# Performance work log

Measured on AMD Instinct MI355X. Metric: run time of the kernel, lower is better.

The kernel has to match this reference:

```python
import jax, jax.numpy as jnp
import numpy as np

NH, NW = 5, 5          # attn_neighborhood_size (odd -> symmetric 'same' padding)
HEADS, HEAD_DIM = 8, 64
DIM = 512              # == heads*head_dim, but project_out=True since heads>1
B, HMAP, WMAP = 4, 64, 64
N = HMAP * WMAP


def local_expand(t, height, width):
    """Equivalent of impulse-filter conv2d neighbor gather.

    t: [b, heads, n, d] -> [b, heads, n, NH*NW, d]
    neighbor f=(i,j) of pixel (p,q) is t[p+i-NH//2, q+j-NW//2], zero-padded.
    """
    b, h, n, d = t.shape
    y = t.reshape(b, h, height, width, d)
    ph, pw = NH // 2, NW // 2
    yp = jnp.pad(y, ((0, 0), (0, 0), (ph, ph), (pw, pw), (0, 0)))
    # fixed small loop over the 25 window offsets (row-major = filter order)
    slabs = [yp[:, :, i:i + height, j:j + width, :]
             for i in range(NH) for j in range(NW)]
    out = jnp.stack(slabs, axis=4)  # [b, h, H, W, F, d]
    return out.reshape(b, h, n, NH * NW, d)


def setup_inputs() -> dict:
    key = jax.random.key(0)
    k1, k2, k3, k4 = jax.random.split(key, 4)
    inner = HEADS * HEAD_DIM
    x = jax.random.normal(k1, (B, N, DIM), dtype=jnp.float32)
    # torch Linear weights are [out_features, in_features]
    w_qkv = jax.random.normal(k2, (3 * inner, DIM), dtype=jnp.float32) * (DIM ** -0.5)
    w_out = jax.random.normal(k3, (DIM, inner), dtype=jnp.float32) * (inner ** -0.5)
    b_out = jax.random.normal(k4, (DIM,), dtype=jnp.float32) * 0.01
    return {"x": x, "w_qkv": w_qkv, "w_out": w_out, "b_out": b_out,
            "h": HMAP, "w": WMAP}


def reference(x, w_qkv, w_out, b_out, h, w):
    b, n, _ = x.shape
    scale = HEAD_DIM ** -0.5
    qkv = x @ w_qkv.T                                   # [b, n, 3*inner]
    q, k, v = jnp.split(qkv, 3, axis=-1)
    def to_heads(t):
        return t.reshape(b, n, HEADS, HEAD_DIM).transpose(0, 2, 1, 3)  # b h n d
    q, k, v = to_heads(q), to_heads(k), to_heads(v)
    k_loc = local_expand(k, h, w)                       # [b, h, n, F, d]
    v_loc = local_expand(v, h, w)
    dots = jnp.einsum('bhnd,bhnfd->bhnf', q, k_loc) * scale
    attn = jax.nn.softmax(dots, axis=-1)
    out = jnp.einsum('bhnf,bhnfd->bhnd', attn, v_loc)   # [b, h, n, d]
    out = out.transpose(0, 2, 1, 3).reshape(b, n, HEADS * HEAD_DIM)
    return out @ w_out.T + b_out                        # dropout=0 (eval)
```

## Files before the change

kernel.cpp:

```cpp
#include <hip/hip_runtime.h>
#include <cstddef>
#include <cstdint>


namespace {

typedef short s16x8 __attribute__((ext_vector_type(8)));
typedef unsigned short u16x8 __attribute__((ext_vector_type(8)));
typedef float f32x4 __attribute__((ext_vector_type(4)));

constexpr int kHeads = 8;
constexpr int kN = 4096;
constexpr float kScale = 0.125f;

__device__ inline float b2f(unsigned short u) {
  return __uint_as_float((unsigned)u << 16);
}
__device__ inline unsigned short f2b(float x) {
  unsigned u = __float_as_uint(x);
  return (unsigned short)((u + 0x7fffu + ((u >> 16) & 1u)) >> 16);
}

__device__ __forceinline__ void g2l16(const unsigned short* g,
                                      unsigned short* l) {
  __builtin_amdgcn_global_load_lds(
      (const __attribute__((address_space(1))) void*)g,
      (__attribute__((address_space(3))) void*)l, 16, 0, 0);
}

__global__ __launch_bounds__(256) void cvt_all(
    const float* __restrict__ wq, const float* __restrict__ wo,
    const float* __restrict__ x, unsigned short* __restrict__ wqb,
    unsigned short* __restrict__ wob, unsigned short* __restrict__ xb) {
  const int i = blockIdx.x * 256 + threadIdx.x;
  const float* src;
  unsigned short* dst;
  int off;
  if (i < 98304) {
    src = wq; dst = wqb; off = i;
  } else if (i < 131072) {
    src = wo; dst = wob; off = i - 98304;
  } else {
    src = x; dst = xb; off = i - 131072;
  }
  const float4 a = ((const float4*)src)[off * 2];
  const float4 b = ((const float4*)src)[off * 2 + 1];
  u16x8 o;
  o[0] = f2b(a.x); o[1] = f2b(a.y); o[2] = f2b(a.z); o[3] = f2b(a.w);
  o[4] = f2b(b.x); o[5] = f2b(b.y); o[6] = f2b(b.z); o[7] = f2b(b.w);
  *(u16x8*)(dst + (size_t)off * 8) = o;
}

__device__ __forceinline__ void mfma_512(const unsigned short* __restrict__ A,
                                         const unsigned short* __restrict__ W,
                                         int m0, int n0, int tid,
                                         unsigned short* As, unsigned short* Bs,
                                         f32x4 (&acc)[4][4]) {
  const int lane = tid & 63;
  const int wv = tid >> 6;
  const int wm = wv & 1, wn = wv >> 1;
  const int rsub = lane >> 3;
  const int slog = (lane & 7) ^ rsub;
#pragma unroll
  for (int i = 0; i < 4; ++i)
#pragma unroll
    for (int j = 0; j < 4; ++j) acc[i][j] = f32x4{0.f, 0.f, 0.f, 0.f};

  for (int k0 = 0; k0 < 512; k0 += 64) {
#pragma unroll
    for (int it = 0; it < 4; ++it) {
      const int g = wv * 4 + it;
      const int row = g * 8 + rsub;
      g2l16(A + (size_t)(m0 + row) * 512 + k0 + slog * 8, As + g * 512);
      g2l16(W + (size_t)(n0 + row) * 512 + k0 + slog * 8, Bs + g * 512);
    }
    __syncthreads();
#pragma unroll
    for (int kh = 0; kh < 2; ++kh) {
      s16x8 af[4], bf[4];
      const int q = kh * 4 + (lane >> 4);
#pragma unroll
      for (int i = 0; i < 4; ++i) {
        const int Ra = wm * 64 + i * 16 + (lane & 15);
        af[i] = *(const s16x8*)&As[Ra * 64 + ((q ^ (Ra & 7)) * 8)];
        const int Rb = wn * 64 + i * 16 + (lane & 15);
        bf[i] = *(const s16x8*)&Bs[Rb * 64 + ((q ^ (Rb & 7)) * 8)];
      }
#pragma unroll
      for (int i = 0; i < 4; ++i)
#pragma unroll
        for (int j = 0; j < 4; ++j)
          acc[i][j] = __builtin_amdgcn_mfma_f32_16x16x32_bf16(
              af[i], bf[j], acc[i][j], 0, 0, 0);
    }
    __syncthreads();
  }
}

__global__ __launch_bounds__(256, 3) void gemm_qkv(
    const unsigned short* __restrict__ A, const unsigned short* __restrict__ W,
    unsigned short* __restrict__ Qb, unsigned short* __restrict__ Kb,
    unsigned short* __restrict__ Vb) {
  __shared__ unsigned short As[8192], Bs[8192];
  const int tid = threadIdx.x;
  const int id = blockIdx.x;
  const int xcd = id & 7;
  const int j = id >> 3;
  const int by = xcd * 16 + j / 12;
  const int bx = j % 12;
  f32x4 acc[4][4];
  mfma_512(A, W, by * 128, bx * 128, tid, As, Bs, acc);

  const int lane = tid & 63;
  const int wv = tid >> 6;
  const int wm = wv & 1, wn = wv >> 1;
  const int cn = bx * 128 + wn * 64;
  unsigned short* dst = (cn < 512) ? Qb : (cn < 1024 ? Kb : Vb);
  const int head = (cn >> 6) & 7;
  const int colb = lane & 15;
#pragma unroll
  for (int mi = 0; mi < 4; ++mi) {
#pragma unroll
    for (int r = 0; r < 4; ++r) {
      const int m = by * 128 + wm * 64 + mi * 16 + (lane >> 4) * 4 + r;
      const int b = m >> 12;
      const int p = m & 4095;
      unsigned short* o =
          dst + ((size_t)(b * kHeads + head) * kN + p) * 64 + colb;
#pragma unroll
      for (int ni = 0; ni < 4; ++ni) o[ni * 16] = f2b(acc[mi][ni][r]);
    }
  }
}

__global__ __launch_bounds__(256, 3) void gemm_out(
    const unsigned short* __restrict__ A, const unsigned short* __restrict__ W,
    const float* __restrict__ bias, float* __restrict__ out) {
  __shared__ unsigned short As[8192], Bs[8192];
  const int tid = threadIdx.x;
  const int id = blockIdx.x;
  const int xcd = id & 7;
  const int j = id >> 3;
  const int by = xcd * 16 + (j >> 2);
  const int bx = j & 3;
  f32x4 acc[4][4];
  mfma_512(A, W, by * 128, bx * 128, tid, As, Bs, acc);

  const int lane = tid & 63;
  const int wv = tid >> 6;
  const int wm = wv & 1, wn = wv >> 1;
  float bvr[4];
#pragma unroll
  for (int ni = 0; ni < 4; ++ni)
    bvr[ni] = bias[bx * 128 + wn * 64 + ni * 16 + (lane & 15)];
#pragma unroll
  for (int mi = 0; mi < 4; ++mi) {
#pragma unroll
    for (int r = 0; r < 4; ++r) {
      const int m = by * 128 + wm * 64 + mi * 16 + (lane >> 4) * 4 + r;
      float* o = out + (size_t)m * 512 + bx * 128 + wn * 64 + (lane & 15);
#pragma unroll
      for (int ni = 0; ni < 4; ++ni) o[ni * 16] = acc[mi][ni][r] + bvr[ni];
    }
  }
}

__global__ __launch_bounds__(512) void attn_p2(
    const unsigned short* __restrict__ Q, const unsigned short* __restrict__ K,
    const unsigned short* __restrict__ V, unsigned short* __restrict__ AO) {
  __shared__ unsigned short H[400 * 72];
  const int tid = threadIdx.x;
  const int bh = blockIdx.y;
  const int tile = blockIdx.x;
  const int ty0 = (tile >> 2) * 16, tx0 = (tile & 3) * 16;
  const size_t base = (size_t)bh * kN;
  const int pix = tid >> 1;
  const int dh = tid & 1;
  const int pyl = pix >> 4, pxl = pix & 15;
  const int p = (ty0 + pyl) * 64 + tx0 + pxl;

  for (int i = tid; i < 3200; i += 512) {
    const int r = i >> 3, c = i & 7;
    const int gy = ty0 - 2 + r / 20;
    const int gx = tx0 - 2 + r % 20;
    u16x8 v = {};
    if ((unsigned)gy < 64u && (unsigned)gx < 64u)
      v = *(const u16x8*)(K + (base + gy * 64 + gx) * 64 + c * 8);
    *(u16x8*)&H[r * 72 + c * 8] = v;
  }
  __syncthreads();

  float dots[25];
#pragma unroll
  for (int f = 0; f < 25; ++f) dots[f] = 0.f;

  const unsigned short* qp = Q + (base + p) * 64 + dh * 32;
#pragma unroll 1
  for (int c = 0; c < 2; ++c) {
    float qv[16];
    {
      const u16x8 a = *(const u16x8*)(qp + c * 16);
      const u16x8 b = *(const u16x8*)(qp + c * 16 + 8);
#pragma unroll
      for (int j = 0; j < 8; ++j) {
        qv[j] = b2f(a[j]);
        qv[8 + j] = b2f(b[j]);
      }
    }
#pragma unroll
    for (int fy = 0; fy < 5; ++fy) {
#pragma unroll
      for (int fx = 0; fx < 5; ++fx) {
        const unsigned short* kr =
            &H[((pyl + fy) * 20 + pxl + fx) * 72 + dh * 32 + c * 16];
        const u16x8 a = *(const u16x8*)kr;
        const u16x8 b = *(const u16x8*)(kr + 8);
        float d = dots[fy * 5 + fx];
#pragma unroll
        for (int j = 0; j < 8; ++j) d = fmaf(qv[j], b2f(a[j]), d);
#pragma unroll
        for (int j = 0; j < 8; ++j) d = fmaf(qv[8 + j], b2f(b[j]), d);
        dots[fy * 5 + fx] = d;
      }
    }
  }

#pragma unroll
  for (int f = 0; f < 25; ++f) dots[f] += __shfl_xor(dots[f], 1, 64);

  float mx = -1e30f;
#pragma unroll
  for (int f = 0; f < 25; ++f) {
    dots[f] *= kScale;
    mx = fmaxf(mx, dots[f]);
  }
  float sum = 0.f;
#pragma unroll
  for (int f = 0; f < 25; ++f) {
    dots[f] = __expf(dots[f] - mx);
    sum += dots[f];
  }
  const float inv = 1.f / sum;
#pragma unroll
  for (int f = 0; f < 25; ++f) dots[f] *= inv;

  __syncthreads();
  for (int i = tid; i < 3200; i += 512) {
    const int r = i >> 3, c = i & 7;
    const int gy = ty0 - 2 + r / 20;
    const int gx = tx0 - 2 + r % 20;
    u16x8 v = {};
    if ((unsigned)gy < 64u && (unsigned)gx < 64u)
      v = *(const u16x8*)(V + (base + gy * 64 + gx) * 64 + c * 8);
    *(u16x8*)&H[r * 72 + c * 8] = v;
  }
  __syncthreads();

  const int b = bh >> 3, h = bh & 7;
  unsigned short* op = AO + ((size_t)(b * kN + p)) * 512 + h * 64 + dh * 32;
#pragma unroll 1
  for (int c = 0; c < 2; ++c) {
    float o[16];
#pragma unroll
    for (int j = 0; j < 16; ++j) o[j] = 0.f;
#pragma unroll
    for (int fy = 0; fy < 5; ++fy) {
#pragma unroll
      for (int fx = 0; fx < 5; ++fx) {
        const unsigned short* vr =
            &H[((pyl + fy) * 20 + pxl + fx) * 72 + dh * 32 + c * 16];
        const u16x8 a = *(const u16x8*)vr;
        const u16x8 b2 = *(const u16x8*)(vr + 8);
        const float wf = dots[fy * 5 + fx];
#pragma unroll
        for (int j = 0; j < 8; ++j) o[j] = fmaf(wf, b2f(a[j]), o[j]);
#pragma unroll
        for (int j = 0; j < 8; ++j) o[8 + j] = fmaf(wf, b2f(b2[j]), o[8 + j]);
      }
    }
    u16x8 pa, pb;
#pragma unroll
    for (int j = 0; j < 8; ++j) {
      pa[j] = f2b(o[j]);
      pb[j] = f2b(o[8 + j]);
    }
    *(u16x8*)(op + c * 16) = pa;
    *(u16x8*)(op + c * 16 + 8) = pb;
  }
}

}

extern "C" void kernel_launch(void* const* d_in, const int* in_sizes, int n_in,
                              void* d_out, int out_size, void* d_ws,
                              size_t ws_size, hipStream_t stream) {
  (void)in_sizes; (void)n_in; (void)out_size; (void)ws_size;
  const float* x = (const float*)d_in[0];
  const float* w_qkv = (const float*)d_in[1];
  const float* w_out = (const float*)d_in[2];
  const float* b_out = (const float*)d_in[3];
  float* out = (float*)d_out;

  unsigned short* ws0 = (unsigned short*)d_ws;
  unsigned short* wqkvb = ws0;
  unsigned short* woutb = ws0 + 786432;
  unsigned short* xb = ws0 + 1048576;
  unsigned short* Qb = ws0 + 9437184;
  unsigned short* Kb = ws0 + 17825792;
  unsigned short* Vb = ws0 + 26214400;
  unsigned short* AO = ws0 + 34603008;

  cvt_all<<<4608, 256, 0, stream>>>(w_qkv, w_out, x, wqkvb, woutb, xb);
  gemm_qkv<<<1536, 256, 0, stream>>>(xb, wqkvb, Qb, Kb, Vb);
  attn_p2<<<dim3(16, 32), 512, 0, stream>>>(Qb, Kb, Vb, AO);
  gemm_out<<<512, 256, 0, stream>>>(AO, woutb, b_out, out);
}
```

Baseline: 172.2 us.

## Restructure local attention: 8-row tiles, 4 threads per pixel, bf16 dot2, XOR-swizzled LDS

The neighborhood attention kernel now uses 16x8 pixel tiles with four threads per pixel instead of two. QK dot products use the packed v_dot2_f32_bf16 instruction rather than unpacking to fp32, and the LDS halo buffer drops its padding in favour of an XOR swizzle to avoid bank conflicts. The grid is flattened and remapped so each XCD handles contiguous batch-head slices for L2 locality. Smaller tiles mean more halo overhead (240 rows for 128 pixels versus 400 for 256), and the extra shuffle stage adds cost, in exchange for higher occupancy, fewer conversion ALU ops and less LDS use.

```diff
diff --git a/kernel.cpp b/kernel.cpp
--- a/kernel.cpp
+++ b/kernel.cpp
@@ -16,9 +16,20 @@
 __device__ inline float b2f(unsigned short u) {
   return __uint_as_float((unsigned)u << 16);
 }
+__device__ inline float blo(unsigned u) {
+  return __uint_as_float(u << 16);
+}
+__device__ inline float bhi(unsigned u) {
+  return __uint_as_float(u & 0xffff0000u);
+}
 __device__ inline unsigned short f2b(float x) {
   unsigned u = __float_as_uint(x);
   return (unsigned short)((u + 0x7fffu + ((u >> 16) & 1u)) >> 16);
+}
+
+__device__ __forceinline__ float dot2bf(float d, unsigned a, unsigned b) {
+  asm("v_dot2_f32_bf16 %0, %1, %2, %0" : "+v"(d) : "v"(a), "v"(b));
+  return d;
 }
 
 __device__ __forceinline__ void g2l16(const unsigned short* g,
@@ -165,68 +176,66 @@
   }
 }
 
-__global__ __launch_bounds__(512) void attn_p2(
+__global__ __launch_bounds__(512, 8) void attn_q4(
     const unsigned short* __restrict__ Q, const unsigned short* __restrict__ K,
     const unsigned short* __restrict__ V, unsigned short* __restrict__ AO) {
-  __shared__ unsigned short H[400 * 72];
+  __shared__ unsigned short H[240 * 64];
   const int tid = threadIdx.x;
-  const int bh = blockIdx.y;
-  const int tile = blockIdx.x;
-  const int ty0 = (tile >> 2) * 16, tx0 = (tile & 3) * 16;
+  const int id = blockIdx.x;
+  const int xcd = id & 7;
+  const int k8 = id >> 3;
+  const int bh = xcd * 4 + (k8 >> 5);
+  const int tile = k8 & 31;
+  const int ty0 = (tile >> 2) * 8, tx0 = (tile & 3) * 16;
   const size_t base = (size_t)bh * kN;
-  const int pix = tid >> 1;
-  const int dh = tid & 1;
+  const int pix = tid >> 2;
+  const int sub = tid & 3;
   const int pyl = pix >> 4, pxl = pix & 15;
   const int p = (ty0 + pyl) * 64 + tx0 + pxl;
 
-  for (int i = tid; i < 3200; i += 512) {
+  for (int i = tid; i < 1920; i += 512) {
     const int r = i >> 3, c = i & 7;
     const int gy = ty0 - 2 + r / 20;
     const int gx = tx0 - 2 + r % 20;
     u16x8 v = {};
     if ((unsigned)gy < 64u && (unsigned)gx < 64u)
       v = *(const u16x8*)(K + (base + gy * 64 + gx) * 64 + c * 8);
-    *(u16x8*)&H[r * 72 + c * 8] = v;
+    *(u16x8*)&H[r * 64 + ((c * 8) ^ ((r & 7) << 3))] = v;
   }
   __syncthreads();
 
+  const unsigned short* qp = Q + (base + p) * 64 + sub * 16;
+  const uint4 qa = *(const uint4*)qp;
+  const uint4 qb = *(const uint4*)(qp + 8);
+
   float dots[25];
 #pragma unroll
-  for (int f = 0; f < 25; ++f) dots[f] = 0.f;
-
-  const unsigned short* qp = Q + (base + p) * 64 + dh * 32;
-#pragma unroll 1
-  for (int c = 0; c < 2; ++c) {
-    float qv[16];
-    {
-      const u16x8 a = *(const u16x8*)(qp + c * 16);
-      const u16x8 b = *(const u16x8*)(qp + c * 16 + 8);
-#pragma unroll
-      for (int j = 0; j < 8; ++j) {
-        qv[j] = b2f(a[j]);
-        qv[8 + j] = b2f(b[j]);
-      }
-    }
-#pragma unroll
-    for (int fy = 0; fy < 5; ++fy) {
-#pragma unroll
-      for (int fx = 0; fx < 5; ++fx) {
-        const unsigned short* kr =
-            &H[((pyl + fy) * 20 + pxl + fx) * 72 + dh * 32 + c * 16];
-        const u16x8 a = *(const u16x8*)kr;
-        const u16x8 b = *(const u16x8*)(kr + 8);
-        float d = dots[fy * 5 + fx];
-#pragma unroll
-        for (int j = 0; j < 8; ++j) d = fmaf(qv[j], b2f(a[j]), d);
-#pragma unroll
-        for (int j = 0; j < 8; ++j) d = fmaf(qv[8 + j], b2f(b[j]), d);
-        dots[fy * 5 + fx] = d;
-      }
-    }
-  }
-
-#pragma unroll
-  for (int f = 0; f < 25; ++f) dots[f] += __shfl_xor(dots[f], 1, 64);
+  for (int fy = 0; fy < 5; ++fy) {
+#pragma unroll
+    for (int fx = 0; fx < 5; ++fx) {
+      const int row = (pyl + fy) * 20 + pxl + fx;
+      const int swz = (row & 7) << 3;
+      const unsigned short* hr = &H[row * 64];
+      const uint4 ka = *(const uint4*)(hr + ((sub * 16) ^ swz));
+      const uint4 kb = *(const uint4*)(hr + ((sub * 16 + 8) ^ swz));
+      float d = 0.f;
+      d = dot2bf(d, qa.x, ka.x);
+      d = dot2bf(d, qa.y, ka.y);
+      d = dot2bf(d, qa.z, ka.z);
+      d = dot2bf(d, qa.w, ka.w);
+      d = dot2bf(d, qb.x, kb.x);
+      d = dot2bf(d, qb.y, kb.y);
+      d = dot2bf(d, qb.z, kb.z);
+      d = dot2bf(d, qb.w, kb.w);
+      dots[fy * 5 + fx] = d;
+    }
+  }
+
+#pragma unroll
+  for (int f = 0; f < 25; ++f) {
+    dots[f] += __shfl_xor(dots[f], 1, 64);
+    dots[f] += __shfl_xor(dots[f], 2, 64);
+  }
 
   float mx = -1e30f;
 #pragma unroll
@@ -245,47 +254,47 @@
   for (int f = 0; f < 25; ++f) dots[f] *= inv;
 
   __syncthreads();
-  for (int i = tid; i < 3200; i += 512) {
+  for (int i = tid; i < 1920; i += 512) {
     const int r = i >> 3, c = i & 7;
     const int gy = ty0 - 2 + r / 20;
     const int gx = tx0 - 2 + r % 20;
     u16x8 v = {};
     if ((unsigned)gy < 64u && (unsigned)gx < 64u)
       v = *(const u16x8*)(V + (base + gy * 64 + gx) * 64 + c * 8);
-    *(u16x8*)&H[r * 72 + c * 8] = v;
+    *(u16x8*)&H[r * 64 + ((c * 8) ^ ((r & 7) << 3))] = v;
   }
   __syncthreads();
 
   const int b = bh >> 3, h = bh & 7;
-  unsigned short* op = AO + ((size_t)(b * kN + p)) * 512 + h * 64 + dh * 32;
+  unsigned short* op = AO + ((size_t)(b * kN + p)) * 512 + h * 64 + sub * 16;
 #pragma unroll 1
-  for (int c = 0; c < 2; ++c) {
-    float o[16];
-#pragma unroll
-    for (int j = 0; j < 16; ++j) o[j] = 0.f;
+  for (int hh = 0; hh < 2; ++hh) {
+    float o[8];
+#pragma unroll
+    for (int j = 0; j < 8; ++j) o[j] = 0.f;
 #pragma unroll
     for (int fy = 0; fy < 5; ++fy) {
 #pragma unroll
       for (int fx = 0; fx < 5; ++fx) {
-        const unsigned short* vr =
-            &H[((pyl + fy) * 20 + pxl + fx) * 72 + dh * 32 + c * 16];
-        const u16x8 a = *(const u16x8*)vr;
-        const u16x8 b2 = *(const u16x8*)(vr + 8);
+        const int row = (pyl + fy) * 20 + pxl + fx;
+        const int swz = (row & 7) << 3;
+        const uint4 va =
+            *(const uint4*)&H[row * 64 + ((sub * 16 + hh * 8) ^ swz)];
         const float wf = dots[fy * 5 + fx];
-#pragma unroll
-        for (int j = 0; j < 8; ++j) o[j] = fmaf(wf, b2f(a[j]), o[j]);
-#pragma unroll
-        for (int j = 0; j < 8; ++j) o[8 + j] = fmaf(wf, b2f(b2[j]), o[8 + j]);
+        o[0] = fmaf(wf, blo(va.x), o[0]);
+        o[1] = fmaf(wf, bhi(va.x), o[1]);
+        o[2] = fmaf(wf, blo(va.y), o[2]);
+        o[3] = fmaf(wf, bhi(va.y), o[3]);
+        o[4] = fmaf(wf, blo(va.z), o[4]);
+        o[5] = fmaf(wf, bhi(va.z), o[5]);
+        o[6] = fmaf(wf, blo(va.w), o[6]);
+        o[7] = fmaf(wf, bhi(va.w), o[7]);
       }
     }
-    u16x8 pa, pb;
-#pragma unroll
-    for (int j = 0; j < 8; ++j) {
-      pa[j] = f2b(o[j]);
-      pb[j] = f2b(o[8 + j]);
-    }
-    *(u16x8*)(op + c * 16) = pa;
-    *(u16x8*)(op + c * 16 + 8) = pb;
+    u16x8 pk;
+#pragma unroll
+    for (int j = 0; j < 8; ++j) pk[j] = f2b(o[j]);
+    *(u16x8*)(op + hh * 8) = pk;
   }
 }
 
@@ -312,6 +321,6 @@
 
   cvt_all<<<4608, 256, 0, stream>>>(w_qkv, w_out, x, wqkvb, woutb, xb);
   gemm_qkv<<<1536, 256, 0, stream>>>(xb, wqkvb, Qb, Kb, Vb);
-  attn_p2<<<dim3(16, 32), 512, 0, stream>>>(Qb, Kb, Vb, AO);
+  attn_q4<<<1024, 512, 0, stream>>>(Qb, Kb, Vb, AO);
   gemm_out<<<512, 256, 0, stream>>>(AO, woutb, b_out, out);
 }
```

Measured after the change: 388.7 us. 126% more time.
